# Optimization experiments

Measured on AMD Instinct MI355X. Metric: run time of the kernel, lower is better.

The kernel has to match this reference:

```python
import jax, jax.numpy as jnp
import numpy as np

L, D, F, H = 4, 1024, 2048, 8
DH = D // H
EPS = 1e-5


def setup_inputs() -> dict:
    key = jax.random.key(0)
    ks = jax.random.split(key, 8)
    B, S = 4, 1024
    sd = 1.0 / np.sqrt(D)
    sf = 1.0 / np.sqrt(F)
    return {
        "X": jax.random.normal(ks[0], (B, S, D), jnp.float32),
        "Wq": jax.random.normal(ks[1], (L, D, D), jnp.float32) * sd,
        "Wk": jax.random.normal(ks[2], (L, D, D), jnp.float32) * sd,
        "Wv": jax.random.normal(ks[3], (L, D, D), jnp.float32) * sd,
        "Wg": jax.random.normal(ks[4], (L, D, D), jnp.float32) * sd,
        "Wo": jax.random.normal(ks[5], (L, D, D), jnp.float32) * sd,
        "W1": jax.random.normal(ks[6], (L, D, F), jnp.float32) * sd,
        "W2": jax.random.normal(ks[7], (L, F, D), jnp.float32) * sf,
        "ln_scale": jnp.ones((D,), jnp.float32),
        "ln_bias": jnp.zeros((D,), jnp.float32),
        "gn_scale": jnp.ones((L, D), jnp.float32),
        "gn_bias": jnp.zeros((L, D), jnp.float32),
    }


def _layer_norm(x, scale, bias):
    mu = x.mean(-1, keepdims=True)
    var = x.var(-1, keepdims=True)
    return (x - mu) * jax.lax.rsqrt(var + EPS) * scale + bias


def _rotate(x, cos, sin):
    # x: (B,S,H,DH); cos/sin: (1,S,1,DH//2); rotary pairs (even, odd)
    x1, x2 = x[..., 0::2], x[..., 1::2]
    r1 = x1 * cos - x2 * sin
    r2 = x1 * sin + x2 * cos
    return jnp.stack([r1, r2], axis=-1).reshape(x.shape)


def _decay_matrix(S):
    # D[h,n,m] = gamma_h^(n-m) for n>=m else 0
    gammas = 1.0 - jnp.exp(jnp.linspace(np.log(1 / 32), np.log(1 / 512), H)).astype(jnp.float32)
    n = jnp.arange(S)
    diff = (n[:, None] - n[None, :]).astype(jnp.float32)
    pw = jnp.exp(jnp.clip(diff, 0.0)[None] * jnp.log(gammas)[:, None, None])
    return jnp.where(diff[None] >= 0, pw, 0.0)  # (H,S,S)


def _retention(x, Wq, Wk, Wv, Wg, Wo, gn_s, gn_b, Dm, cos, sin):
    B, S, _ = x.shape
    Q = (x @ Wq).reshape(B, S, H, DH)
    K = (x @ Wk).reshape(B, S, H, DH)
    V = (x @ Wv).reshape(B, S, H, DH)
    Q = _rotate(Q, cos, sin)
    K = _rotate(K, cos, -sin)  # conjugate phase
    att = jnp.einsum('bnhd,bmhd->bhnm', Q, K) * Dm  # (B,H,S,S)
    Y = jnp.einsum('bhnm,bmhd->bnhd', att, V)
    # group norm: normalize each head's output per token
    mu = Y.mean(-1, keepdims=True)
    var = Y.var(-1, keepdims=True)
    Y = (Y - mu) * jax.lax.rsqrt(var + EPS)
    Y = Y.reshape(B, S, D) * gn_s + gn_b
    G = jax.nn.swish(x @ Wg)
    return (G * Y) @ Wo


def reference(X, Wq, Wk, Wv, Wg, Wo, W1, W2, ln_scale, ln_bias, gn_scale, gn_bias):
    B, S, _ = X.shape
    pos = jnp.arange(S, dtype=jnp.float32)
    inv_freq = 1.0 / (10000.0 ** (jnp.arange(0, DH, 2, dtype=jnp.float32) / DH))
    ang = pos[:, None] * inv_freq[None, :]  # (S, DH//2)
    cos = jnp.cos(ang)[None, :, None, :]
    sin = jnp.sin(ang)[None, :, None, :]
    Dm = _decay_matrix(S)
    for i in range(L):
        Yr = _retention(_layer_norm(X, ln_scale, ln_bias), Wq[i], Wk[i], Wv[i],
                        Wg[i], Wo[i], gn_scale[i], gn_bias[i], Dm, cos, sin) + X
        X = jax.nn.gelu(_layer_norm(Yr, ln_scale, ln_bias) @ W1[i]) @ W2[i] + Yr
    return X
```

## Files before the change

kernel.cpp:

```cpp
#include <hip/hip_runtime.h>
#include <hip/hip_bf16.h>
#include <cmath>

#define LAYERS 4
#define Bb 4
#define Ss 1024
#define Dd 1024
#define Ff 2048
#define Hh 8
#define DHd 128
#define Mm (Bb * Ss)
#define EPSf 1e-5f
#define LDQ 4096

typedef __attribute__((ext_vector_type(8))) short short8v;
typedef __attribute__((ext_vector_type(4))) float f32x4;
typedef __attribute__((ext_vector_type(4))) unsigned int u32x4;

__device__ __forceinline__ float swish_f(float x) { return x / (1.f + expf(-x)); }
__device__ __forceinline__ float gelu_f(float x) {
  return 0.5f * x * (1.f + tanhf(0.7978845608028654f * (x + 0.044715f * x * x * x)));
}
__device__ __forceinline__ unsigned short f2bfu(float f) {
  __hip_bfloat16 h = __float2bfloat16(f);
  return __builtin_bit_cast(unsigned short, h);
}
__device__ __forceinline__ float bfu2f(unsigned short u) {
  unsigned v = ((unsigned)u) << 16;
  return __builtin_bit_cast(float, v);
}
__device__ __forceinline__ void gl_lds16(const void* g, void* l) {
  __builtin_amdgcn_global_load_lds((__attribute__((address_space(1))) void*)g,
                                   (__attribute__((address_space(3))) void*)l, 16, 0, 0);
}
__device__ __forceinline__ f32x4 mfma16(short8v a, short8v b, f32x4 c) {
  return __builtin_amdgcn_mfma_f32_16x16x32_bf16(a, b, c, 0, 0, 0);
}

__global__ __launch_bounds__(256) void ln_bf16_kernel(const float* __restrict__ x,
                                                      short* __restrict__ outb,
                                                      const float* __restrict__ sc,
                                                      const float* __restrict__ bi) {
  const int row = blockIdx.x;
  const int t = threadIdx.x;
  const float4 v = *(const float4*)(x + (size_t)row * Dd + t * 4);
  float s = v.x + v.y + v.z + v.w;
  float s2 = v.x * v.x + v.y * v.y + v.z * v.z + v.w * v.w;
#pragma unroll
  for (int o = 32; o > 0; o >>= 1) { s += __shfl_down(s, o); s2 += __shfl_down(s2, o); }
  __shared__ float ps[4], ps2[4];
  if ((t & 63) == 0) { ps[t >> 6] = s; ps2[t >> 6] = s2; }
  __syncthreads();
  s = ps[0] + ps[1] + ps[2] + ps[3];
  s2 = ps2[0] + ps2[1] + ps2[2] + ps2[3];
  const float mu = s * (1.f / Dd);
  const float var = s2 * (1.f / Dd) - mu * mu;
  const float rstd = rsqrtf(var + EPSf);
  const float4 g = *(const float4*)(sc + t * 4);
  const float4 b = *(const float4*)(bi + t * 4);
  const float o0 = (v.x - mu) * rstd * g.x + b.x;
  const float o1 = (v.y - mu) * rstd * g.y + b.y;
  const float o2 = (v.z - mu) * rstd * g.z + b.z;
  const float o3 = (v.w - mu) * rstd * g.w + b.w;
  unsigned p0 = (unsigned)f2bfu(o0) | ((unsigned)f2bfu(o1) << 16);
  unsigned p1 = (unsigned)f2bfu(o2) | ((unsigned)f2bfu(o3) << 16);
  uint2 pk; pk.x = p0; pk.y = p1;
  *(uint2*)(outb + (size_t)row * Dd + t * 4) = pk;
}

__global__ void rope_table_kernel(float* __restrict__ ct, float* __restrict__ st) {
  const int i = blockIdx.x * 256 + threadIdx.x;
  const int s = i >> 6, f = i & 63;
  const float inv = powf(10000.f, -(float)f / 64.f);
  const float a = (float)s * inv;
  ct[i] = cosf(a);
  st[i] = sinf(a);
}

__global__ __launch_bounds__(256) void wtrans_ln_kernel(
    const float* __restrict__ Wq, const float* __restrict__ Wk,
    const float* __restrict__ Wv, const float* __restrict__ Wg,
    const float* __restrict__ Wo, const float* __restrict__ W1,
    const float* __restrict__ W2,
    short* __restrict__ Wqkvgt, short* __restrict__ Wot,
    short* __restrict__ W1t, short* __restrict__ W2t,
    const float* __restrict__ x, short* __restrict__ outb,
    const float* __restrict__ sc, const float* __restrict__ bi) {
  __shared__ float tile[32][33];
  __shared__ float ps[4], ps2[4];
  const int t = threadIdx.x;
  const int blk = blockIdx.x;
  if (blk >= 9216) {
    const int row = blk - 9216;
    const float4 v = *(const float4*)(x + (size_t)row * Dd + t * 4);
    float s = v.x + v.y + v.z + v.w;
    float s2 = v.x * v.x + v.y * v.y + v.z * v.z + v.w * v.w;
#pragma unroll
    for (int o = 32; o > 0; o >>= 1) { s += __shfl_down(s, o); s2 += __shfl_down(s2, o); }
    if ((t & 63) == 0) { ps[t >> 6] = s; ps2[t >> 6] = s2; }
    __syncthreads();
    s = ps[0] + ps[1] + ps[2] + ps[3];
    s2 = ps2[0] + ps2[1] + ps2[2] + ps2[3];
    const float mu = s * (1.f / Dd);
    const float var = s2 * (1.f / Dd) - mu * mu;
    const float rstd = rsqrtf(var + EPSf);
    const float4 g = *(const float4*)(sc + t * 4);
    const float4 b = *(const float4*)(bi + t * 4);
    const float o0 = (v.x - mu) * rstd * g.x + b.x;
    const float o1 = (v.y - mu) * rstd * g.y + b.y;
    const float o2 = (v.z - mu) * rstd * g.z + b.z;
    const float o3 = (v.w - mu) * rstd * g.w + b.w;
    unsigned p0 = (unsigned)f2bfu(o0) | ((unsigned)f2bfu(o1) << 16);
    unsigned p1 = (unsigned)f2bfu(o2) | ((unsigned)f2bfu(o3) << 16);
    uint2 pk; pk.x = p0; pk.y = p1;
    *(uint2*)(outb + (size_t)row * Dd + t * 4) = pk;
    return;
  }
  const int tc = t & 31, tr8 = t >> 5;
  const float* src; short* dst; int K, N, n0, k0, nl;
  if (blk < 4096) {
    const int bx = blk & 127, ky = blk >> 7;
    n0 = bx * 32; k0 = ky * 32;
    const int which = n0 >> 10;
    src = (which == 0) ? Wq : (which == 1) ? Wk : (which == 2) ? Wv : Wg;
    nl = n0 & 1023; N = 1024; K = 1024; dst = Wqkvgt;
  } else if (blk < 5120) {
    const int b2 = blk - 4096;
    n0 = (b2 & 31) * 32; k0 = (b2 >> 5) * 32; nl = n0;
    src = Wo; N = 1024; K = 1024; dst = Wot;
  } else if (blk < 7168) {
    const int b2 = blk - 5120;
    n0 = (b2 & 63) * 32; k0 = (b2 >> 6) * 32; nl = n0;
    src = W1; N = 2048; K = 1024; dst = W1t;
  } else {
    const int b2 = blk - 7168;
    n0 = (b2 & 31) * 32; k0 = (b2 >> 5) * 32; nl = n0;
    src = W2; N = 1024; K = 2048; dst = W2t;
  }
#pragma unroll
  for (int i = 0; i < 4; ++i) {
    const int r = tr8 + i * 8;
    tile[r][tc] = src[(size_t)(k0 + r) * N + nl + tc];
  }
  __syncthreads();
#pragma unroll
  for (int i = 0; i < 4; ++i) {
    const int r = tr8 + i * 8;
    dst[(size_t)(n0 + r) * K + k0 + tc] = (short)f2bfu(tile[tc][r]);
  }
}

__global__ __launch_bounds__(256) void rope_qk_kernel(short* __restrict__ QKVGb,
                                                      const float* __restrict__ ct,
                                                      const float* __restrict__ st) {
  const int idx = blockIdx.x * 256 + threadIdx.x;
  const int f = idx & 63;
  const int h = (idx >> 6) & 7;
  const int r = idx >> 9;
  const int s = r & (Ss - 1);
  const float c = ct[(s << 6) + f], sn = st[(s << 6) + f];
  const size_t qo = (size_t)r * LDQ + h * DHd + 2 * f;
  const unsigned qp = *(const unsigned*)(QKVGb + qo);
  const unsigned kp = *(const unsigned*)(QKVGb + qo + 1024);
  const float qx = bfu2f((unsigned short)(qp & 0xffff)), qy = bfu2f((unsigned short)(qp >> 16));
  const float kx = bfu2f((unsigned short)(kp & 0xffff)), ky = bfu2f((unsigned short)(kp >> 16));
  const unsigned qn = (unsigned)f2bfu(qx * c - qy * sn) |
                      ((unsigned)f2bfu(qx * sn + qy * c) << 16);
  const unsigned kn = (unsigned)f2bfu(kx * c + ky * sn) |
                      ((unsigned)f2bfu(-kx * sn + ky * c) << 16);
  *(unsigned*)(QKVGb + qo) = qn;
  *(unsigned*)(QKVGb + qo + 1024) = kn;
}

template <int EPI>
__global__ __launch_bounds__(512, 2) void gemm10(const short* __restrict__ A,
                                                 const short* __restrict__ Bt,
                                                 float* __restrict__ Cf,
                                                 short* __restrict__ Cb,
                                                 const float* __restrict__ Res,
                                                 short* __restrict__ Vt,
                                                 int N, int K, int ldc) {
  __shared__ __align__(16) short SM[65536];
  const int t = threadIdx.x;
  const int w = t >> 6, l = t & 63;
  const int lq = l >> 4, lr = l & 15;
  const int wr = w >> 2, wc = w & 3;
  const int bhalf = wc >> 1, brow0 = (wc & 1) * 64;
  const int nwg = gridDim.x * gridDim.y;
  const int bid0 = blockIdx.x + blockIdx.y * gridDim.x;
  const int lgid = (bid0 & 7) * (nwg >> 3) + (bid0 >> 3);
  const int bx = lgid % gridDim.x, by = lgid / gridDim.x;
  const int row0 = by * 256, col0 = bx * 256;
  const int NT = K >> 6;

  f32x4 acc[8][4] = {};
  short8v a[4][2], b[4][2];

  auto stageA = [&](int kt, int hf) {
    const int db = kt & 1;
    short* dstb = SM + (db * 2 + hf) * 8192;
#pragma unroll
    for (int i = 0; i < 2; ++i) {
      const int c = t + i * 512;
      const int row = c >> 3, slot = c & 7;
      gl_lds16(A + (size_t)(row0 + hf * 128 + row) * K + kt * 64 + ((slot ^ (row & 7)) << 3),
               dstb + c * 8);
    }
  };
  auto stageB = [&](int kt, int hf) {
    const int db = kt & 1;
    short* dstb = SM + 32768 + (db * 2 + hf) * 8192;
#pragma unroll
    for (int i = 0; i < 2; ++i) {
      const int c = t + i * 512;
      const int row = c >> 3, slot = c & 7;
      gl_lds16(Bt + (size_t)(col0 + hf * 128 + row) * K + kt * 64 + ((slot ^ (row & 7)) << 3),
               dstb + c * 8);
    }
  };
  auto rdA = [&](int db, int m, int ks) -> short8v {
    const int row = m * 16 + lr;
    return *(const short8v*)(SM + (db * 2 + wr) * 8192 + row * 64 +
                             (((ks << 2) + lq) ^ (row & 7)) * 8);
  };
  auto rdB = [&](int db, int n, int ks) -> short8v {
    const int row = brow0 + n * 16 + lr;
    return *(const short8v*)(SM + 32768 + (db * 2 + bhalf) * 8192 + row * 64 +
                             (((ks << 2) + lq) ^ (row & 7)) * 8);
  };

  stageA(0, 0); stageA(0, 1); stageB(0, 0); stageB(0, 1);
  if (NT > 1) { stageB(1, 0); stageB(1, 1); }
  if (NT > 1) { asm volatile("s_waitcnt vmcnt(4)" ::: "memory"); }
  else        { asm volatile("s_waitcnt vmcnt(0)" ::: "memory"); }
  asm volatile("s_barrier" ::: "memory");

  for (int kt = 0; kt < NT; ++kt) {
    const int db = kt & 1;
#pragma unroll
    for (int m = 0; m < 4; ++m) { a[m][0] = rdA(db, m, 0); a[m][1] = rdA(db, m, 1); }
#pragma unroll
    for (int n = 0; n < 2; ++n) { b[n][0] = rdB(db, n, 0); b[n][1] = rdB(db, n, 1); }
    if (kt + 1 < NT) stageA(kt + 1, 0);
    __builtin_amdgcn_s_setprio(1);
#pragma unroll
    for (int m = 0; m < 4; ++m)
#pragma unroll
      for (int n = 0; n < 2; ++n) {
        acc[m][n] = mfma16(a[m][0], b[n][0], acc[m][n]);
        acc[m][n] = mfma16(a[m][1], b[n][1], acc[m][n]);
      }
    __builtin_amdgcn_s_setprio(0);
    asm volatile("s_barrier" ::: "memory");
#pragma unroll
    for (int n = 2; n < 4; ++n) { b[n][0] = rdB(db, n, 0); b[n][1] = rdB(db, n, 1); }
    if (kt + 1 < NT) stageA(kt + 1, 1);
    __builtin_amdgcn_s_setprio(1);
#pragma unroll
    for (int m = 0; m < 4; ++m)
#pragma unroll
      for (int n = 2; n < 4; ++n) {
        acc[m][n] = mfma16(a[m][0], b[n][0], acc[m][n]);
        acc[m][n] = mfma16(a[m][1], b[n][1], acc[m][n]);
      }
    __builtin_amdgcn_s_setprio(0);
    asm volatile("s_barrier" ::: "memory");
#pragma unroll
    for (int m = 0; m < 4; ++m) { a[m][0] = rdA(db, m + 4, 0); a[m][1] = rdA(db, m + 4, 1); }
    if (kt + 2 < NT) stageB(kt + 2, 0);
    __builtin_amdgcn_s_setprio(1);
#pragma unroll
    for (int m = 0; m < 4; ++m)
#pragma unroll
      for (int n = 0; n < 2; ++n) {
        acc[m + 4][n] = mfma16(a[m][0], b[n][0], acc[m + 4][n]);
        acc[m + 4][n] = mfma16(a[m][1], b[n][1], acc[m + 4][n]);
      }
    __builtin_amdgcn_s_setprio(0);
    asm volatile("s_barrier" ::: "memory");
    if (kt + 2 < NT) stageB(kt + 2, 1);
    __builtin_amdgcn_s_setprio(1);
#pragma unroll
    for (int m = 0; m < 4; ++m)
#pragma unroll
      for (int n = 2; n < 4; ++n) {
        acc[m + 4][n] = mfma16(a[m][0], b[n][0], acc[m + 4][n]);
        acc[m + 4][n] = mfma16(a[m][1], b[n][1], acc[m + 4][n]);
      }
    __builtin_amdgcn_s_setprio(0);
    if (kt + 2 < NT) { asm volatile("s_waitcnt vmcnt(4)" ::: "memory"); }
    else             { asm volatile("s_waitcnt vmcnt(0)" ::: "memory"); }
    asm volatile("s_barrier" ::: "memory");
  }

  if (EPI == 0 && col0 >= 2048 && col0 < 3072) {
#pragma unroll
    for (int m = 0; m < 8; ++m)
#pragma unroll
      for (int n = 0; n < 4; ++n)
#pragma unroll
        for (int r = 0; r < 4; ++r) {
          const int ls = wr * 128 + m * 16 + lq * 4 + r;
          const int ld = wc * 64 + n * 16 + lr;
          SM[ld * 256 + ((((ls >> 3) ^ (ld & 31)) << 3) | (ls & 7))] =
              (short)f2bfu(acc[m][n][r]);
        }
    __syncthreads();
    const int bI = row0 >> 10;
    const int s0g = row0 & 1023;
#pragma unroll 4
    for (int rr = 0; rr < 32; ++rr) {
      const int dl = w * 32 + rr;
      const int gcol = (col0 - 2048) + dl;
      const int hh = gcol >> 7, dh = gcol & 127;
      unsigned pk0, pk1;
      {
        const int s0 = l * 4;
        const unsigned short e0 =
            (unsigned short)SM[dl * 256 + ((((s0 + 0) >> 3) ^ (dl & 31)) << 3 | ((s0 + 0) & 7))];
        const unsigned short e1 =
            (unsigned short)SM[dl * 256 + ((((s0 + 1) >> 3) ^ (dl & 31)) << 3 | ((s0 + 1) & 7))];
        const unsigned short e2 =
            (unsigned short)SM[dl * 256 + ((((s0 + 2) >> 3) ^ (dl & 31)) << 3 | ((s0 + 2) & 7))];
        const unsigned short e3 =
            (unsigned short)SM[dl * 256 + ((((s0 + 3) >> 3) ^ (dl & 31)) << 3 | ((s0 + 3) & 7))];
        pk0 = (unsigned)e0 | ((unsigned)e1 << 16);
        pk1 = (unsigned)e2 | ((unsigned)e3 << 16);
      }
      uint2 pk; pk.x = pk0; pk.y = pk1;
      *(uint2*)(Vt + ((size_t)((bI * 8 + hh) * 128 + dh)) * Ss + s0g + l * 4) = pk;
    }
    return;
  }

#pragma unroll
  for (int m = 0; m < 8; ++m) {
#pragma unroll
    for (int n = 0; n < 4; ++n) {
#pragma unroll
      for (int r = 0; r < 4; ++r) {
        const int row = row0 + wr * 128 + m * 16 + lq * 4 + r;
        const int col = col0 + wc * 64 + n * 16 + lr;
        const size_t o = (size_t)row * ldc + col;
        float v = acc[m][n][r];
        if (EPI == 0) Cb[o] = (short)f2bfu(v);
        else if (EPI == 1) Cf[o] = v + Res[o];
        else Cb[o] = (short)f2bfu(gelu_f(v));
      }
    }
  }
}

template <int EPI>
__global__ __launch_bounds__(512) void gemm11(const short* __restrict__ A,
                                              const short* __restrict__ Bt,
                                              float* __restrict__ Cf,
                                              short* __restrict__ Cb,
                                              const float* __restrict__ Res,
                                              int K, int lda, int ldb, int ldc, int nxt) {
  __shared__ __align__(16) short As[3][256 * 64];
  __shared__ __align__(16) short Bs[3][128 * 64];
  const int t = threadIdx.x;
  const int w = t >> 6, l = t & 63;
  const int lq = l >> 4, lr = l & 15;
  const int wr = w >> 2, wc = w & 3;
  const int nwg = gridDim.x;
  const int lgid = (blockIdx.x & 7) * (nwg >> 3) + (blockIdx.x >> 3);
  const int mt = lgid / nxt, nt_ = lgid % nxt;
  const int row0 = mt * 256, col0 = nt_ * 128;
  const int NT = K >> 6;
  f32x4 acc[8][2] = {};
  short8v a[4][2], b[2][2];

  auto stageA = [&](int kt, int hf) {
    const int s = kt % 3;
#pragma unroll
    for (int i = 0; i < 2; ++i) {
      const int c = t + i * 512;
      const int row = c >> 3, slot = c & 7;
      gl_lds16(A + (size_t)(row0 + hf * 128 + row) * lda + kt * 64 + ((slot ^ (row & 7)) << 3),
               &As[s][hf * 8192 + c * 8]);
    }
  };
  auto stageB = [&](int kt) {
    const int s = kt % 3;
#pragma unroll
    for (int i = 0; i < 2; ++i) {
      const int c = t + i * 512;
      const int row = c >> 3, slot = c & 7;
      gl_lds16(Bt + (size_t)(col0 + row) * ldb + kt * 64 + ((slot ^ (row & 7)) << 3),
               &Bs[s][c * 8]);
    }
  };
  auto rdA = [&](int s, int m, int ks) -> short8v {
    const int row = wr * 128 + m * 16 + lr;
    return *(const short8v*)&As[s][row * 64 + (((ks << 2) + lq) ^ (row & 7)) * 8];
  };
  auto rdB = [&](int s, int n, int ks) -> short8v {
    const int row = wc * 32 + n * 16 + lr;
    return *(const short8v*)&Bs[s][row * 64 + (((ks << 2) + lq) ^ (row & 7)) * 8];
  };

  stageA(0, 0); stageA(0, 1); stageB(0);
  stageA(1, 0); stageA(1, 1); stageB(1);
  asm volatile("s_waitcnt vmcnt(6)" ::: "memory");
  asm volatile("s_barrier" ::: "memory");

  for (int kt = 0; kt < NT; ++kt) {
    const int s = kt % 3;
#pragma unroll
    for (int m = 0; m < 4; ++m) { a[m][0] = rdA(s, m, 0); a[m][1] = rdA(s, m, 1); }
#pragma unroll
    for (int n = 0; n < 2; ++n) { b[n][0] = rdB(s, n, 0); b[n][1] = rdB(s, n, 1); }
    if (kt + 2 < NT) stageA(kt + 2, 0);
    __builtin_amdgcn_s_setprio(1);
#pragma unroll
    for (int m = 0; m < 4; ++m)
#pragma unroll
      for (int n = 0; n < 2; ++n) {
        acc[m][n] = mfma16(a[m][0], b[n][0], acc[m][n]);
        acc[m][n] = mfma16(a[m][1], b[n][1], acc[m][n]);
      }
    __builtin_amdgcn_s_setprio(0);
    asm volatile("s_barrier" ::: "memory");
#pragma unroll
    for (int m = 0; m < 4; ++m) { a[m][0] = rdA(s, m + 4, 0); a[m][1] = rdA(s, m + 4, 1); }
    if (kt + 2 < NT) { stageA(kt + 2, 1); stageB(kt + 2); }
    __builtin_amdgcn_s_setprio(1);
#pragma unroll
    for (int m = 0; m < 4; ++m)
#pragma unroll
      for (int n = 0; n < 2; ++n) {
        acc[m + 4][n] = mfma16(a[m][0], b[n][0], acc[m + 4][n]);
        acc[m + 4][n] = mfma16(a[m][1], b[n][1], acc[m + 4][n]);
      }
    __builtin_amdgcn_s_setprio(0);
    if (kt + 2 < NT) { asm volatile("s_waitcnt vmcnt(6)" ::: "memory"); }
    else             { asm volatile("s_waitcnt vmcnt(0)" ::: "memory"); }
    asm volatile("s_barrier" ::: "memory");
  }

#pragma unroll
  for (int m = 0; m < 8; ++m) {
#pragma unroll
    for (int n = 0; n < 2; ++n) {
#pragma unroll
      for (int r = 0; r < 4; ++r) {
        const int row = row0 + wr * 128 + m * 16 + lq * 4 + r;
        const int col = col0 + wc * 32 + n * 16 + lr;
        const size_t o = (size_t)row * ldc + col;
        float v = acc[m][n][r];
        if (EPI == 0) Cb[o] = (short)f2bfu(v);
        else if (EPI == 1) Cf[o] = v + Res[o];
        else Cb[o] = (short)f2bfu(gelu_f(v));
      }
    }
  }
}

template <int EPI>
__global__ __launch_bounds__(512) void gemm12(const short* __restrict__ A,
                                              const short* __restrict__ Bt,
                                              float* __restrict__ Cf,
                                              short* __restrict__ Cb,
                                              const float* __restrict__ Res,
                                              int K, int lda, int ldb, int ldc, int nxt) {
  __shared__ __align__(16) short As[3][128 * 64];
  __shared__ __align__(16) short Bs[3][128 * 64];
  const int t = threadIdx.x;
  const int w = t >> 6, l = t & 63;
  const int lq = l >> 4, lr = l & 15;
  const int wr = w >> 2, wc = w & 3;
  const int nwg = gridDim.x;
  const int lgid = (blockIdx.x & 7) * (nwg >> 3) + (blockIdx.x >> 3);
  const int mt = lgid / nxt, nt_ = lgid % nxt;
  const int row0 = mt * 128, col0 = nt_ * 128;
  const int NT = K >> 6;
  f32x4 acc[4][2] = {};
  short8v a[4][2], b[2][2];

  auto stageA = [&](int kt) {
    const int s = kt % 3;
#pragma unroll
    for (int i = 0; i < 2; ++i) {
      const int c = t + i * 512;
      const int row = c >> 3, slot = c & 7;
      gl_lds16(A + (size_t)(row0 + row) * lda + kt * 64 + ((slot ^ (row & 7)) << 3),
               &As[s][c * 8]);
    }
  };
  auto stageB = [&](int kt) {
    const int s = kt % 3;
#pragma unroll
    for (int i = 0; i < 2; ++i) {
      const int c = t + i * 512;
      const int row = c >> 3, slot = c & 7;
      gl_lds16(Bt + (size_t)(col0 + row) * ldb + kt * 64 + ((slot ^ (row & 7)) << 3),
               &Bs[s][c * 8]);
    }
  };
  auto rdA = [&](int s, int m, int ks) -> short8v {
    const int row = wr * 64 + m * 16 + lr;
    return *(const short8v*)&As[s][row * 64 + (((ks << 2) + lq) ^ (row & 7)) * 8];
  };
  auto rdB = [&](int s, int n, int ks) -> short8v {
    const int row = wc * 32 + n * 16 + lr;
    return *(const short8v*)&Bs[s][row * 64 + (((ks << 2) + lq) ^ (row & 7)) * 8];
  };

  stageA(0); stageB(0);
  stageA(1); stageB(1);
  asm volatile("s_waitcnt vmcnt(4)" ::: "memory");
  asm volatile("s_barrier" ::: "memory");

  for (int kt = 0; kt < NT; ++kt) {
    const int s = kt % 3;
#pragma unroll
    for (int m = 0; m < 4; ++m) { a[m][0] = rdA(s, m, 0); a[m][1] = rdA(s, m, 1); }
#pragma unroll
    for (int n = 0; n < 2; ++n) { b[n][0] = rdB(s, n, 0); b[n][1] = rdB(s, n, 1); }
    if (kt + 2 < NT) stageA(kt + 2);
    __builtin_amdgcn_s_setprio(1);
#pragma unroll
    for (int m = 0; m < 2; ++m)
#pragma unroll
      for (int n = 0; n < 2; ++n) {
        acc[m][n] = mfma16(a[m][0], b[n][0], acc[m][n]);
        acc[m][n] = mfma16(a[m][1], b[n][1], acc[m][n]);
      }
    __builtin_amdgcn_s_setprio(0);
    asm volatile("s_barrier" ::: "memory");
    if (kt + 2 < NT) stageB(kt + 2);
    __builtin_amdgcn_s_setprio(1);
#pragma unroll
    for (int m = 2; m < 4; ++m)
#pragma unroll
      for (int n = 0; n < 2; ++n) {
        acc[m][n] = mfma16(a[m][0], b[n][0], acc[m][n]);
        acc[m][n] = mfma16(a[m][1], b[n][1], acc[m][n]);
      }
    __builtin_amdgcn_s_setprio(0);
    if (kt + 2 < NT) { asm volatile("s_waitcnt vmcnt(4)" ::: "memory"); }
    else             { asm volatile("s_waitcnt vmcnt(0)" ::: "memory"); }
    asm volatile("s_barrier" ::: "memory");
  }

#pragma unroll
  for (int m = 0; m < 4; ++m) {
#pragma unroll
    for (int n = 0; n < 2; ++n) {
#pragma unroll
      for (int r = 0; r < 4; ++r) {
        const int row = row0 + wr * 64 + m * 16 + lq * 4 + r;
        const int col = col0 + wc * 32 + n * 16 + lr;
        const size_t o = (size_t)row * ldc + col;
        float v = acc[m][n][r];
        if (EPI == 0) Cb[o] = (short)f2bfu(v);
        else if (EPI == 1) Cf[o] = v + Res[o];
        else Cb[o] = (short)f2bfu(gelu_f(v));
      }
    }
  }
}

__global__ __launch_bounds__(256) void ret5_kernel(const short* __restrict__ QKVGb,
                                                   const short* __restrict__ Vt,
                                                   short* __restrict__ Gb,
                                                   const float* __restrict__ gs,
                                                   const float* __restrict__ gb) {
  __shared__ __align__(16) short Ks[2][64 * 128];
  __shared__ __align__(16) short Vs[2][128 * 64];
  const int t = threadIdx.x, w = t >> 6, l = t & 63;
  const int lq = l >> 4, lr = l & 15;
  const int u = blockIdx.x;
  const int lgid = (u & 7) * 32 + (u >> 3);
  const int bh = lgid >> 3, pr = lgid & 7;
  const int b = bh >> 3, h = bh & 7;
  const float lstep = (logf(1.f / 512.f) - logf(1.f / 32.f)) * (1.f / 7.f);
  const float gamma = 1.f - expf(logf(1.f / 32.f) + (float)h * lstep);
  const float l2g = logf(gamma) * 1.44269504f;
  const short* Qp = QKVGb;
  const short* Kp = QKVGb + 1024;

  float cmf[4], csr[4];
#pragma unroll
  for (int mf = 0; mf < 4; ++mf) cmf[mf] = exp2f(l2g * (float)(-16 * mf));
#pragma unroll
  for (int r = 0; r < 4; ++r) csr[r] = exp2f(l2g * (float)(63 - 4 * lq - r));
  float gsv[8], gbv[8];
#pragma unroll
  for (int nd = 0; nd < 8; ++nd) {
    gsv[nd] = gs[h * DHd + nd * 16 + lr];
    gbv[nd] = gb[h * DHd + nd * 16 + lr];
  }
  const int sb = ((lq & 1) * 2) * 16 + lr;

  auto stageKV = [&](int m0, int buf) {
#pragma unroll
    for (int i = 0; i < 4; ++i) {
      const int c = (w * 4 + i) * 64 + l;
      const int row = c >> 4, slot = c & 15;
      gl_lds16(Kp + (size_t)(b * Ss + m0 + row) * LDQ + h * DHd + ((slot ^ (row & 7)) * 8),
               &Ks[buf][(w * 4 + i) * 512]);
    }
#pragma unroll
    for (int i = 0; i < 4; ++i) {
      const int c = (w * 4 + i) * 64 + l;
      const int row = c >> 3, slot = c & 7;
      gl_lds16(Vt + (size_t)(bh * DHd + row) * Ss + m0 + ((slot ^ (row & 7)) * 8),
               &Vs[buf][(w * 4 + i) * 512]);
    }
  };

  for (int pass = 0; pass < 2; ++pass) {
    const int qb = pass ? (15 - pr) : pr;
    const int q0 = qb * 64;
    const int nt = qb + 1;
    short8v qf[4];
#pragma unroll
    for (int ks = 0; ks < 4; ++ks)
      qf[ks] = *(const short8v*)(Qp + (size_t)(b * Ss + q0 + w * 16 + lr) * LDQ +
                                 h * DHd + ks * 32 + lq * 8);
    f32x4 yacc[8] = {};
    stageKV(0, 0);
    __syncthreads();
    int cur = 0;
    for (int tt = 0; tt < nt; ++tt) {
      const int m0 = tt * 64;
      if (tt + 1 < nt) stageKV((tt + 1) * 64, cur ^ 1);

      f32x4 st[4] = {};
      __builtin_amdgcn_s_setprio(1);
#pragma unroll
      for (int mf = 0; mf < 4; ++mf) {
        const int row = mf * 16 + lr;
#pragma unroll
        for (int ks = 0; ks < 4; ++ks) {
          short8v kf = *(const short8v*)&Ks[cur][row * 128 + (((4 * ks + lq) ^ (row & 7)) * 8)];
          st[mf] = mfma16(kf, qf[ks], st[mf]);
        }
      }
      __builtin_amdgcn_s_setprio(0);
      const int qg = q0 + w * 16 + lr;
      const float rs = exp2f(l2g * (float)(qg - m0 - 63));
#pragma unroll
      for (int mf = 0; mf < 4; ++mf)
#pragma unroll
        for (int r = 0; r < 4; ++r) {
          const int kvg = m0 + mf * 16 + lq * 4 + r;
          const float wgt = (qg >= kvg) ? rs * cmf[mf] * csr[r] : 0.f;
          st[mf][r] *= wgt;
        }
      unsigned pk[4][2];
#pragma unroll
      for (int mf = 0; mf < 4; ++mf)
#pragma unroll
        for (int p = 0; p < 2; ++p)
          pk[mf][p] = (unsigned)f2bfu(st[mf][2 * p]) |
                      ((unsigned)f2bfu(st[mf][2 * p + 1]) << 16);
      short8v afr[2];
#pragma unroll
      for (int ks2 = 0; ks2 < 2; ++ks2) {
        u32x4 wd;
#pragma unroll
        for (int wj = 0; wj < 4; ++wj) {
          const int src = sb + (wj >> 1) * 16;
          const unsigned v0 = __shfl(pk[2 * ks2 + 0][wj & 1], src);
          const unsigned v1 = __shfl(pk[2 * ks2 + 1][wj & 1], src);
          wd[wj] = (lq >= 2) ? v1 : v0;
        }
        afr[ks2] = __builtin_bit_cast(short8v, wd);
      }
      __builtin_amdgcn_s_setprio(1);
#pragma unroll
      for (int nd = 0; nd < 8; ++nd) {
        const int row = nd * 16 + lr;
#pragma unroll
        for (int ks2 = 0; ks2 < 2; ++ks2) {
          short8v vf = *(const short8v*)&Vs[cur][row * 64 + (((4 * ks2 + lq) ^ (row & 7)) * 8)];
          yacc[nd] = mfma16(afr[ks2], vf, yacc[nd]);
        }
      }
      __builtin_amdgcn_s_setprio(0);
      __syncthreads();
      cur ^= 1;
    }
#pragma unroll
    for (int r = 0; r < 4; ++r) {
      float s1 = 0.f, s2 = 0.f;
#pragma unroll
      for (int nd = 0; nd < 8; ++nd) { const float v = yacc[nd][r]; s1 += v; s2 += v * v; }
#pragma unroll
      for (int msk = 1; msk < 16; msk <<= 1) {
        s1 += __shfl_xor(s1, msk);
        s2 += __shfl_xor(s2, msk);
      }
      const float mu = s1 * (1.f / 128.f);
      const float rstd = rsqrtf(s2 * (1.f / 128.f) - mu * mu + EPSf);
      const int q = q0 + w * 16 + lq * 4 + r;
      const size_t gbase = (size_t)(b * Ss + q) * LDQ + 3072 + h * DHd;
      const size_t obase = (size_t)(b * Ss + q) * Dd + h * DHd;
#pragma unroll
      for (int nd = 0; nd < 8; ++nd) {
        const int d = nd * 16 + lr;
        const float yv = (yacc[nd][r] - mu) * rstd * gsv[nd] + gbv[nd];
        const float gvx = bfu2f((unsigned short)QKVGb[gbase + d]);
        Gb[obase + d] = (short)f2bfu(swish_f(gvx) * yv);
      }
    }
  }
}

extern "C" void kernel_launch(void* const* d_in, const int* in_sizes, int n_in,
                              void* d_out, int out_size, void* d_ws, size_t ws_size,
                              hipStream_t stream) {
  const float* X = (const float*)d_in[0];
  const float* Wq = (const float*)d_in[1];
  const float* Wk = (const float*)d_in[2];
  const float* Wv = (const float*)d_in[3];
  const float* Wg = (const float*)d_in[4];
  const float* Wo = (const float*)d_in[5];
  const float* W1 = (const float*)d_in[6];
  const float* W2 = (const float*)d_in[7];
  const float* lns = (const float*)d_in[8];
  const float* lnb = (const float*)d_in[9];
  const float* gns = (const float*)d_in[10];
  const float* gnb = (const float*)d_in[11];
  float* out = (float*)d_out;

  char* W = (char*)d_ws;
  const size_t MB = 1u << 20;
  float* Abuf  = (float*)(W);
  short* Xnb   = (short*)(W + 16 * MB);
  short* QKVGb = (short*)(W + 24 * MB);
  short* Vtb   = (short*)(W + 88 * MB);
  short* Gb    = (short*)(W + 96 * MB);
  short* Wqkvgt= (short*)(W + 104 * MB);
  short* Wot   = (short*)(W + 112 * MB);
  short* W1t   = (short*)(W + 114 * MB);
  short* W2t   = (short*)(W + 118 * MB);
  float* ct    = (float*)(W + 122 * MB);
  float* st    = ct + Ss * 64;
  short* Hb = QKVGb;

  rope_table_kernel<<<(Ss * 64) / 256, 256, 0, stream>>>(ct, st);

  for (int l = 0; l < LAYERS; ++l) {
    const size_t DD = (size_t)Dd * Dd;
    const float* Acur = (l == 0) ? X : Abuf;
    wtrans_ln_kernel<<<13312, 256, 0, stream>>>(Wq + l * DD, Wk + l * DD, Wv + l * DD,
                                                Wg + l * DD, Wo + l * DD,
                                                W1 + (size_t)l * Dd * Ff,
                                                W2 + (size_t)l * Ff * Dd,
                                                Wqkvgt, Wot, W1t, W2t,
                                                Acur, Xnb, lns, lnb);
    gemm10<0><<<dim3(16, 16), 512, 0, stream>>>(Xnb, Wqkvgt, nullptr, QKVGb,
                                                nullptr, Vtb, 4096, Dd, LDQ);
    rope_qk_kernel<<<8192, 256, 0, stream>>>(QKVGb, ct, st);
    ret5_kernel<<<256, 256, 0, stream>>>(QKVGb, Vtb, Gb,
                                         gns + (size_t)l * Dd, gnb + (size_t)l * Dd);
    gemm12<1><<<256, 512, 0, stream>>>(Gb, Wot, Abuf, nullptr, Acur,
                                       Dd, Dd, Dd, Dd, 8);
    ln_bf16_kernel<<<Mm, 256, 0, stream>>>(Abuf, Xnb, lns, lnb);
    gemm11<2><<<256, 512, 0, stream>>>(Xnb, W1t, nullptr, Hb, nullptr,
                                       Dd, Dd, Dd, Ff, 16);
    float* dst = (l == LAYERS - 1) ? out : Abuf;
    gemm12<1><<<256, 512, 0, stream>>>(Hb, W2t, dst, nullptr, Abuf,
                                       Ff, Ff, Ff, Dd, 8);
  }
}
```

Before: 685.4 us.

## Fuse rotary embedding of Q and K into the retention kernel

Removes the standalone RoPE kernel and applies the rotation inside the retention kernel. Q fragments are rotated in registers after loading, and K tiles are loaded through registers, rotated, and written to LDS, replacing the direct global-to-LDS copy. This saves one read/write pass over the Q and K regions per layer, plus a kernel launch. In exchange, K is rotated redundantly for every query block, and the K staging now goes through registers, which adds register pressure and VALU work inside the pipelined loop.

```diff
diff --git a/kernel.cpp b/kernel.cpp
--- a/kernel.cpp
+++ b/kernel.cpp
@@ -148,28 +148,6 @@
     const int r = tr8 + i * 8;
     dst[(size_t)(n0 + r) * K + k0 + tc] = (short)f2bfu(tile[tc][r]);
   }
-}
-
-__global__ __launch_bounds__(256) void rope_qk_kernel(short* __restrict__ QKVGb,
-                                                      const float* __restrict__ ct,
-                                                      const float* __restrict__ st) {
-  const int idx = blockIdx.x * 256 + threadIdx.x;
-  const int f = idx & 63;
-  const int h = (idx >> 6) & 7;
-  const int r = idx >> 9;
-  const int s = r & (Ss - 1);
-  const float c = ct[(s << 6) + f], sn = st[(s << 6) + f];
-  const size_t qo = (size_t)r * LDQ + h * DHd + 2 * f;
-  const unsigned qp = *(const unsigned*)(QKVGb + qo);
-  const unsigned kp = *(const unsigned*)(QKVGb + qo + 1024);
-  const float qx = bfu2f((unsigned short)(qp & 0xffff)), qy = bfu2f((unsigned short)(qp >> 16));
-  const float kx = bfu2f((unsigned short)(kp & 0xffff)), ky = bfu2f((unsigned short)(kp >> 16));
-  const unsigned qn = (unsigned)f2bfu(qx * c - qy * sn) |
-                      ((unsigned)f2bfu(qx * sn + qy * c) << 16);
-  const unsigned kn = (unsigned)f2bfu(kx * c + ky * sn) |
-                      ((unsigned)f2bfu(-kx * sn + ky * c) << 16);
-  *(unsigned*)(QKVGb + qo) = qn;
-  *(unsigned*)(QKVGb + qo + 1024) = kn;
 }
 
 template <int EPI>
@@ -563,11 +541,13 @@
   }
 }
 
-__global__ __launch_bounds__(256) void ret5_kernel(const short* __restrict__ QKVGb,
+__global__ __launch_bounds__(256) void ret6_kernel(const short* __restrict__ QKVGb,
                                                    const short* __restrict__ Vt,
                                                    short* __restrict__ Gb,
                                                    const float* __restrict__ gs,
-                                                   const float* __restrict__ gb) {
+                                                   const float* __restrict__ gb,
+                                                   const float* __restrict__ ct,
+                                                   const float* __restrict__ st) {
   __shared__ __align__(16) short Ks[2][64 * 128];
   __shared__ __align__(16) short Vs[2][128 * 64];
   const int t = threadIdx.x, w = t >> 6, l = t & 63;
@@ -595,14 +575,41 @@
   }
   const int sb = ((lq & 1) * 2) * 16 + lr;
 
-  auto stageKV = [&](int m0, int buf) {
+  uint4 kreg[4];
+  float4 kct[4], kst[4];
+  auto ldK = [&](int m0) {
 #pragma unroll
     for (int i = 0; i < 4; ++i) {
       const int c = (w * 4 + i) * 64 + l;
       const int row = c >> 4, slot = c & 15;
-      gl_lds16(Kp + (size_t)(b * Ss + m0 + row) * LDQ + h * DHd + ((slot ^ (row & 7)) * 8),
-               &Ks[buf][(w * 4 + i) * 512]);
-    }
+      const int sch = slot ^ (row & 7);
+      kreg[i] = *(const uint4*)(Kp + (size_t)(b * Ss + m0 + row) * LDQ + h * DHd + sch * 8);
+      const int sp = m0 + row;
+      kct[i] = *(const float4*)&ct[(sp << 6) + sch * 4];
+      kst[i] = *(const float4*)&st[(sp << 6) + sch * 4];
+    }
+  };
+  auto writeK = [&](int buf) {
+#pragma unroll
+    for (int i = 0; i < 4; ++i) {
+      const float cc[4] = {kct[i].x, kct[i].y, kct[i].z, kct[i].w};
+      const float ss[4] = {kst[i].x, kst[i].y, kst[i].z, kst[i].w};
+      unsigned uu[4] = {kreg[i].x, kreg[i].y, kreg[i].z, kreg[i].w};
+      uint4 outv;
+      unsigned ov[4];
+#pragma unroll
+      for (int j = 0; j < 4; ++j) {
+        const float lo = bfu2f((unsigned short)(uu[j] & 0xffff));
+        const float hi = bfu2f((unsigned short)(uu[j] >> 16));
+        const float nl = lo * cc[j] + hi * ss[j];
+        const float nh = -lo * ss[j] + hi * cc[j];
+        ov[j] = (unsigned)f2bfu(nl) | ((unsigned)f2bfu(nh) << 16);
+      }
+      outv.x = ov[0]; outv.y = ov[1]; outv.z = ov[2]; outv.w = ov[3];
+      *(uint4*)&Ks[buf][(w * 4 + i) * 512 + l * 8] = outv;
+    }
+  };
+  auto stageV = [&](int m0, int buf) {
 #pragma unroll
     for (int i = 0; i < 4; ++i) {
       const int c = (w * 4 + i) * 64 + l;
@@ -616,20 +623,35 @@
     const int qb = pass ? (15 - pr) : pr;
     const int q0 = qb * 64;
     const int nt = qb + 1;
+    const int spq = q0 + w * 16 + lr;
     short8v qf[4];
 #pragma unroll
-    for (int ks = 0; ks < 4; ++ks)
-      qf[ks] = *(const short8v*)(Qp + (size_t)(b * Ss + q0 + w * 16 + lr) * LDQ +
+    for (int ks = 0; ks < 4; ++ks) {
+      qf[ks] = *(const short8v*)(Qp + (size_t)(b * Ss + spq) * LDQ +
                                  h * DHd + ks * 32 + lq * 8);
+      const float4 c4 = *(const float4*)&ct[(spq << 6) + ks * 16 + lq * 4];
+      const float4 s4 = *(const float4*)&st[(spq << 6) + ks * 16 + lq * 4];
+      const float cc[4] = {c4.x, c4.y, c4.z, c4.w};
+      const float ssn[4] = {s4.x, s4.y, s4.z, s4.w};
+#pragma unroll
+      for (int j = 0; j < 4; ++j) {
+        const float lo = bfu2f((unsigned short)qf[ks][2 * j]);
+        const float hi = bfu2f((unsigned short)qf[ks][2 * j + 1]);
+        qf[ks][2 * j]     = (short)f2bfu(lo * cc[j] - hi * ssn[j]);
+        qf[ks][2 * j + 1] = (short)f2bfu(lo * ssn[j] + hi * cc[j]);
+      }
+    }
     f32x4 yacc[8] = {};
-    stageKV(0, 0);
+    ldK(0);
+    stageV(0, 0);
+    writeK(0);
     __syncthreads();
     int cur = 0;
     for (int tt = 0; tt < nt; ++tt) {
       const int m0 = tt * 64;
-      if (tt + 1 < nt) stageKV((tt + 1) * 64, cur ^ 1);
-
-      f32x4 st[4] = {};
+      if (tt + 1 < nt) { ldK((tt + 1) * 64); stageV((tt + 1) * 64, cur ^ 1); }
+
+      f32x4 stv[4] = {};
       __builtin_amdgcn_s_setprio(1);
 #pragma unroll
       for (int mf = 0; mf < 4; ++mf) {
@@ -637,27 +659,26 @@
 #pragma unroll
         for (int ks = 0; ks < 4; ++ks) {
           short8v kf = *(const short8v*)&Ks[cur][row * 128 + (((4 * ks + lq) ^ (row & 7)) * 8)];
-          st[mf] = mfma16(kf, qf[ks], st[mf]);
+          stv[mf] = mfma16(kf, qf[ks], stv[mf]);
         }
       }
       __builtin_amdgcn_s_setprio(0);
-      const int qg = q0 + w * 16 + lr;
-      const float rs = exp2f(l2g * (float)(qg - m0 - 63));
+      const float rs = exp2f(l2g * (float)(spq - m0 - 63));
 #pragma unroll
       for (int mf = 0; mf < 4; ++mf)
 #pragma unroll
         for (int r = 0; r < 4; ++r) {
           const int kvg = m0 + mf * 16 + lq * 4 + r;
-          const float wgt = (qg >= kvg) ? rs * cmf[mf] * csr[r] : 0.f;
-          st[mf][r] *= wgt;
+          const float wgt = (spq >= kvg) ? rs * cmf[mf] * csr[r] : 0.f;
+          stv[mf][r] *= wgt;
         }
       unsigned pk[4][2];
 #pragma unroll
       for (int mf = 0; mf < 4; ++mf)
 #pragma unroll
         for (int p = 0; p < 2; ++p)
-          pk[mf][p] = (unsigned)f2bfu(st[mf][2 * p]) |
-                      ((unsigned)f2bfu(st[mf][2 * p + 1]) << 16);
+          pk[mf][p] = (unsigned)f2bfu(stv[mf][2 * p]) |
+                      ((unsigned)f2bfu(stv[mf][2 * p + 1]) << 16);
       short8v afr[2];
 #pragma unroll
       for (int ks2 = 0; ks2 < 2; ++ks2) {
@@ -682,6 +703,7 @@
         }
       }
       __builtin_amdgcn_s_setprio(0);
+      if (tt + 1 < nt) writeK(cur ^ 1);
       __syncthreads();
       cur ^= 1;
     }
@@ -708,6 +730,7 @@
         Gb[obase + d] = (short)f2bfu(swish_f(gvx) * yv);
       }
     }
+    if (pass == 0) __syncthreads();
   }
 }
 
@@ -756,9 +779,9 @@
                                                 Acur, Xnb, lns, lnb);
     gemm10<0><<<dim3(16, 16), 512, 0, stream>>>(Xnb, Wqkvgt, nullptr, QKVGb,
                                                 nullptr, Vtb, 4096, Dd, LDQ);
-    rope_qk_kernel<<<8192, 256, 0, stream>>>(QKVGb, ct, st);
-    ret5_kernel<<<256, 256, 0, stream>>>(QKVGb, Vtb, Gb,
-                                         gns + (size_t)l * Dd, gnb + (size_t)l * Dd);
+    ret6_kernel<<<256, 256, 0, stream>>>(QKVGb, Vtb, Gb,
+                                         gns + (size_t)l * Dd, gnb + (size_t)l * Dd,
+                                         ct, st);
     gemm12<1><<<256, 512, 0, stream>>>(Gb, Wot, Abuf, nullptr, Acur,
                                        Dd, Dd, Dd, Dd, 8);
     ln_bf16_kernel<<<Mm, 256, 0, stream>>>(Abuf, Xnb, lns, lnb);
```

Measured after the change: 708.8 us. 1.03x slower.

## Overlap next-layer weight transpose with retention kernel via extra blocks

Applied to the files above, without the earlier changes.

The retention kernel launch gains 9216 extra blocks that transpose and convert the next layer's weights to bf16 into a double-buffered weight area. Only 256 blocks do retention work, so the spare compute units can convert weights at the same time. The separate fused weight-transpose plus layernorm kernel now runs only for layer 0, and later layers use a plain layernorm kernel. The workspace layout is packed tighter to make room for two weight buffers. The risk is that the transpose blocks compete with the retention blocks for memory bandwidth and scheduling slots.

```diff
diff --git a/kernel.cpp b/kernel.cpp
--- a/kernel.cpp
+++ b/kernel.cpp
@@ -563,14 +563,56 @@
   }
 }
 
-__global__ __launch_bounds__(256) void ret5_kernel(const short* __restrict__ QKVGb,
-                                                   const short* __restrict__ Vt,
-                                                   short* __restrict__ Gb,
-                                                   const float* __restrict__ gs,
-                                                   const float* __restrict__ gb) {
+__global__ __launch_bounds__(256) void ret5w_kernel(
+    const short* __restrict__ QKVGb, const short* __restrict__ Vt,
+    short* __restrict__ Gb, const float* __restrict__ gs, const float* __restrict__ gb,
+    const float* __restrict__ Wq, const float* __restrict__ Wk,
+    const float* __restrict__ Wv, const float* __restrict__ Wg,
+    const float* __restrict__ Wo, const float* __restrict__ W1,
+    const float* __restrict__ W2,
+    short* __restrict__ dWqkvg, short* __restrict__ dWo,
+    short* __restrict__ dW1, short* __restrict__ dW2) {
   __shared__ __align__(16) short Ks[2][64 * 128];
   __shared__ __align__(16) short Vs[2][128 * 64];
-  const int t = threadIdx.x, w = t >> 6, l = t & 63;
+  const int t = threadIdx.x;
+  if (blockIdx.x >= 256) {
+    float (*tile)[33] = (float(*)[33]) & Ks[0][0];
+    const int blk = blockIdx.x - 256;
+    const int tc = t & 31, tr8 = t >> 5;
+    const float* src; short* dst; int K, N, n0, k0, nl;
+    if (blk < 4096) {
+      const int bx = blk & 127, ky = blk >> 7;
+      n0 = bx * 32; k0 = ky * 32;
+      const int which = n0 >> 10;
+      src = (which == 0) ? Wq : (which == 1) ? Wk : (which == 2) ? Wv : Wg;
+      nl = n0 & 1023; N = 1024; K = 1024; dst = dWqkvg;
+    } else if (blk < 5120) {
+      const int b2 = blk - 4096;
+      n0 = (b2 & 31) * 32; k0 = (b2 >> 5) * 32; nl = n0;
+      src = Wo; N = 1024; K = 1024; dst = dWo;
+    } else if (blk < 7168) {
+      const int b2 = blk - 5120;
+      n0 = (b2 & 63) * 32; k0 = (b2 >> 6) * 32; nl = n0;
+      src = W1; N = 2048; K = 1024; dst = dW1;
+    } else {
+      const int b2 = blk - 7168;
+      n0 = (b2 & 31) * 32; k0 = (b2 >> 5) * 32; nl = n0;
+      src = W2; N = 1024; K = 2048; dst = dW2;
+    }
+#pragma unroll
+    for (int i = 0; i < 4; ++i) {
+      const int r = tr8 + i * 8;
+      tile[r][tc] = src[(size_t)(k0 + r) * N + nl + tc];
+    }
+    __syncthreads();
+#pragma unroll
+    for (int i = 0; i < 4; ++i) {
+      const int r = tr8 + i * 8;
+      dst[(size_t)(n0 + r) * K + k0 + tc] = (short)f2bfu(tile[tc][r]);
+    }
+    return;
+  }
+  const int w = t >> 6, l = t & 63;
   const int lq = l >> 4, lr = l & 15;
   const int u = blockIdx.x;
   const int lgid = (u & 7) * 32 + (u >> 3);
@@ -733,39 +775,56 @@
   float* Abuf  = (float*)(W);
   short* Xnb   = (short*)(W + 16 * MB);
   short* QKVGb = (short*)(W + 24 * MB);
-  short* Vtb   = (short*)(W + 88 * MB);
-  short* Gb    = (short*)(W + 96 * MB);
-  short* Wqkvgt= (short*)(W + 104 * MB);
-  short* Wot   = (short*)(W + 112 * MB);
-  short* W1t   = (short*)(W + 114 * MB);
-  short* W2t   = (short*)(W + 118 * MB);
-  float* ct    = (float*)(W + 122 * MB);
+  short* Vtb   = (short*)(W + 56 * MB);
+  short* Gb    = (short*)(W + 64 * MB);
+  short* Wqkvgt0 = (short*)(W + 72 * MB);
+  short* Wot0    = (short*)(W + 80 * MB);
+  short* W1t0    = (short*)(W + 82 * MB);
+  short* W2t0    = (short*)(W + 86 * MB);
+  short* Wqkvgt1 = (short*)(W + 90 * MB);
+  short* Wot1    = (short*)(W + 98 * MB);
+  short* W1t1    = (short*)(W + 100 * MB);
+  short* W2t1    = (short*)(W + 104 * MB);
+  float* ct    = (float*)(W + 108 * MB);
   float* st    = ct + Ss * 64;
   short* Hb = QKVGb;
 
+  short* WqkvgtB[2] = {Wqkvgt0, Wqkvgt1};
+  short* WotB[2]    = {Wot0, Wot1};
+  short* W1tB[2]    = {W1t0, W1t1};
+  short* W2tB[2]    = {W2t0, W2t1};
+
   rope_table_kernel<<<(Ss * 64) / 256, 256, 0, stream>>>(ct, st);
 
   for (int l = 0; l < LAYERS; ++l) {
     const size_t DD = (size_t)Dd * Dd;
+    const int cb = l & 1;
     const float* Acur = (l == 0) ? X : Abuf;
-    wtrans_ln_kernel<<<13312, 256, 0, stream>>>(Wq + l * DD, Wk + l * DD, Wv + l * DD,
-                                                Wg + l * DD, Wo + l * DD,
-                                                W1 + (size_t)l * Dd * Ff,
-                                                W2 + (size_t)l * Ff * Dd,
-                                                Wqkvgt, Wot, W1t, W2t,
-                                                Acur, Xnb, lns, lnb);
-    gemm10<0><<<dim3(16, 16), 512, 0, stream>>>(Xnb, Wqkvgt, nullptr, QKVGb,
+    if (l == 0) {
+      wtrans_ln_kernel<<<13312, 256, 0, stream>>>(Wq, Wk, Wv, Wg, Wo, W1, W2,
+                                                  Wqkvgt0, Wot0, W1t0, W2t0,
+                                                  Acur, Xnb, lns, lnb);
+    } else {
+      ln_bf16_kernel<<<Mm, 256, 0, stream>>>(Acur, Xnb, lns, lnb);
+    }
+    gemm10<0><<<dim3(16, 16), 512, 0, stream>>>(Xnb, WqkvgtB[cb], nullptr, QKVGb,
                                                 nullptr, Vtb, 4096, Dd, LDQ);
     rope_qk_kernel<<<8192, 256, 0, stream>>>(QKVGb, ct, st);
-    ret5_kernel<<<256, 256, 0, stream>>>(QKVGb, Vtb, Gb,
-                                         gns + (size_t)l * Dd, gnb + (size_t)l * Dd);
-    gemm12<1><<<256, 512, 0, stream>>>(Gb, Wot, Abuf, nullptr, Acur,
+    const int ln = (l + 1 < LAYERS) ? (l + 1) : l;
+    const int grid_ret = (l + 1 < LAYERS) ? (256 + 9216) : 256;
+    ret5w_kernel<<<grid_ret, 256, 0, stream>>>(
+        QKVGb, Vtb, Gb, gns + (size_t)l * Dd, gnb + (size_t)l * Dd,
+        Wq + (size_t)ln * DD, Wk + (size_t)ln * DD, Wv + (size_t)ln * DD,
+        Wg + (size_t)ln * DD, Wo + (size_t)ln * DD,
+        W1 + (size_t)ln * Dd * Ff, W2 + (size_t)ln * Ff * Dd,
+        WqkvgtB[cb ^ 1], WotB[cb ^ 1], W1tB[cb ^ 1], W2tB[cb ^ 1]);
+    gemm12<1><<<256, 512, 0, stream>>>(Gb, WotB[cb], Abuf, nullptr, Acur,
                                        Dd, Dd, Dd, Dd, 8);
     ln_bf16_kernel<<<Mm, 256, 0, stream>>>(Abuf, Xnb, lns, lnb);
-    gemm11<2><<<256, 512, 0, stream>>>(Xnb, W1t, nullptr, Hb, nullptr,
+    gemm11<2><<<256, 512, 0, stream>>>(Xnb, W1tB[cb], nullptr, Hb, nullptr,
                                        Dd, Dd, Dd, Ff, 16);
     float* dst = (l == LAYERS - 1) ? out : Abuf;
-    gemm12<1><<<256, 512, 0, stream>>>(Hb, W2t, dst, nullptr, Abuf,
+    gemm12<1><<<256, 512, 0, stream>>>(Hb, W2tB[cb], dst, nullptr, Abuf,
                                        Ff, Ff, Ff, Dd, 8);
   }
 }
```

Result: no change. 696.3 us (+1.6%).
